# Kernel tuning notes

Measured on AMD Instinct MI355X. Metric: run time of the kernel, lower is better.

The kernel has to match this reference:

```python
import jax, jax.numpy as jnp
import numpy as np

EMBED_DIM = 512
SMOOTH = 4.0        # args.lambda_softmax
LAMBDA_LSE = 6.0    # args.lambda_lse
LEAKY_SLOPE = 0.1
EPS = 1e-8


def setup_inputs() -> dict:
    key = jax.random.key(0)
    k1, k2, k3 = jax.random.split(key, 3)
    n_contract, n_region = 32, 256
    n_law, max_len = 32, 256
    contracts = jax.random.normal(k1, (n_contract, n_region, EMBED_DIM), jnp.float32)
    laws = jax.random.normal(k2, (n_law, max_len, EMBED_DIM), jnp.float32)
    law_lens = jax.random.randint(k3, (n_law,), 128, max_len + 1, jnp.int32)
    return {"contracts": contracts, "laws": laws, "law_lens": law_lens}


def reference(contracts, laws, law_lens):
    # contracts: [C, R, D], laws: [N, L, D], law_lens: [N]
    n_law, max_len, d = laws.shape
    # mask[n, l] = 1 if word l is within law n's true length
    mask = (jnp.arange(max_len)[None, :] < law_lens[:, None]).astype(contracts.dtype)

    # attn = law @ contract^T / sqrt(D): [N, C, L, R]
    attn = jnp.einsum('nld,crd->nclr', laws, contracts) / jnp.sqrt(jnp.float32(d))
    attn = jax.nn.leaky_relu(attn, LEAKY_SLOPE)
    # l2norm over region dim (per law-word row)
    attn = attn / (jnp.linalg.norm(attn, axis=-1, keepdims=True) + EPS)
    attn = jax.nn.softmax(attn, axis=-1) * SMOOTH
    # zero out contributions from padded law words (ragged lengths)
    attn = attn * mask[:, None, :, None]

    # weighted_law: [N, C, R, D]
    wlaw = jnp.einsum('nld,nclr->ncrd', laws, attn)

    # cosine similarity along D: [N, C, R]
    w12 = jnp.sum(contracts[None] * wlaw, axis=-1)
    w1 = jnp.linalg.norm(contracts, axis=-1)[None]          # [1, C, R]
    w2 = jnp.linalg.norm(wlaw, axis=-1)                      # [N, C, R]
    sim = w12 / jnp.maximum(w1 * w2, EPS)

    # LogSumExp aggregation over regions -> [N, C]
    row_sim = jnp.log(jnp.sum(jnp.exp(sim * LAMBDA_LSE), axis=-1)) / LAMBDA_LSE
    # concatenate per-law columns -> [C, N]
    return row_sim.T
```

## Files before the change

### kernel.cpp

```cpp
#include <hip/hip_runtime.h>
#include <hip/hip_bf16.h>

#define CN 32
#define RN 256
#define DN 512
#define NN 32
#define LN 256

#define STAGE_OFF 131072
#define SMEM_TOTAL 163840

typedef short v8s __attribute__((ext_vector_type(8)));
typedef float v4f __attribute__((ext_vector_type(4)));
typedef const __attribute__((address_space(1))) void* gas1_t;
typedef __attribute__((address_space(3))) void* las3_t;

__device__ __forceinline__ void gl2lds16(const void* g, void* l) {
  __builtin_amdgcn_global_load_lds((gas1_t)g, (las3_t)l, 16, 0, 0);
}

__device__ __forceinline__ unsigned short f2bf(float x) {
  unsigned int u = __float_as_uint(x);
  u = (u + 0x7fffu + ((u >> 16) & 1u)) >> 16;
  return (unsigned short)u;
}
__device__ __forceinline__ float bf2f(unsigned short h) {
  return __uint_as_float(((unsigned int)h) << 16);
}

__device__ __forceinline__ const v8s* stgFrag(const unsigned short* buf, int r,
                                              int quad) {
  return (const v8s*)(buf + r * 32 + ((quad ^ ((r >> 1) & 3)) << 3));
}

__device__ __forceinline__ int satIdx(int r, int col) {
  return (r << 8) | ((((col >> 3) ^ (r & 7)) << 3) | (col & 7));
}

__global__ __launch_bounds__(256) void prep_kernel(
    const float* __restrict__ con, const float* __restrict__ laws,
    unsigned short* __restrict__ lawsB, unsigned short* __restrict__ conB,
    float* __restrict__ cnorm) {
  const int b = blockIdx.x;
  const int t = threadIdx.x;
  const int base = b * DN;
  float a0 = laws[base + t], a1 = laws[base + t + 256];
  lawsB[base + t] = f2bf(a0);
  lawsB[base + t + 256] = f2bf(a1);
  float c0 = con[base + t], c1 = con[base + t + 256];
  conB[base + t] = f2bf(c0);
  conB[base + t + 256] = f2bf(c1);
  float s = c0 * c0 + c1 * c1;
#pragma unroll
  for (int m = 1; m < 64; m <<= 1) s += __shfl_xor(s, m, 64);
  __shared__ float r4[4];
  if ((t & 63) == 0) r4[t >> 6] = s;
  __syncthreads();
  if (t == 0) cnorm[b] = sqrtf(r4[0] + r4[1] + r4[2] + r4[3]);
}

__global__ __launch_bounds__(512) void gramm_kernel(
    const unsigned short* __restrict__ lawsB, unsigned short* __restrict__ G) {
  __shared__ unsigned short lawsAll[256 * 32];
  __shared__ unsigned short lawsSub[64 * 32];
  const int bx = blockIdx.x;
  const int n = bx >> 2;
  const int m0 = (bx & 3) << 6;
  const int t = threadIdx.x;
  const int lane = t & 63;
  const int w = t >> 6;
  const int quad = lane >> 4;
  const int l16 = lane & 15;
  const int sub = t & 3;
  const int rQ = t >> 2;
  const int subx = sub ^ ((rQ >> 1) & 3);
  const unsigned short* lawN = lawsB + n * (LN * DN);
  const int wr = (w & 1) << 5;
  const int wc = (w >> 1) << 6;

  v4f acc[2][4];
#pragma unroll
  for (int a = 0; a < 2; ++a)
#pragma unroll
    for (int b = 0; b < 4; ++b) acc[a][b] = (v4f){0.f, 0.f, 0.f, 0.f};

  for (int ch = 0; ch < 16; ++ch) {
    const int dk = ch << 5;
    __syncthreads();
#pragma unroll
    for (int i = 0; i < 2; ++i)
      gl2lds16(lawN + (i * 128 + rQ) * DN + dk + subx * 8,
               (char*)lawsAll + i * 8192 + t * 16);
    if (t < 256)
      gl2lds16(lawN + (m0 + rQ) * DN + dk + subx * 8, (char*)lawsSub + t * 16);
    __syncthreads();
    v8s af0 = *stgFrag(lawsSub, wr + l16, quad);
    v8s af1 = *stgFrag(lawsSub, wr + 16 + l16, quad);
#pragma unroll
    for (int rt = 0; rt < 4; ++rt) {
      v8s bf = *stgFrag(lawsAll, wc + rt * 16 + l16, quad);
      acc[0][rt] = __builtin_amdgcn_mfma_f32_16x16x32_bf16(af0, bf, acc[0][rt], 0, 0, 0);
      acc[1][rt] = __builtin_amdgcn_mfma_f32_16x16x32_bf16(af1, bf, acc[1][rt], 0, 0, 0);
    }
  }
  unsigned short* g = G + n * (LN * LN);
#pragma unroll
  for (int tl = 0; tl < 2; ++tl)
#pragma unroll
    for (int reg = 0; reg < 4; ++reg) {
      const int l = m0 + wr + tl * 16 + quad * 4 + reg;
#pragma unroll
      for (int rt = 0; rt < 4; ++rt)
        g[l * LN + wc + rt * 16 + l16] = f2bf(acc[tl][rt][reg]);
    }
}

__global__ __launch_bounds__(512, 2) void main_kernel(
    const int* __restrict__ law_lens, const unsigned short* __restrict__ lawsB,
    const unsigned short* __restrict__ conB, const unsigned short* __restrict__ Gm,
    const float* __restrict__ cnorm, float* __restrict__ out) {
  extern __shared__ char smem[];
  unsigned short* sAt = (unsigned short*)smem;
  char* stage = smem + STAGE_OFF;

  const int bid = blockIdx.x;
  const int n = bid >> 5;
  const int c = bid & 31;
  const int t = threadIdx.x;
  const int lane = t & 63;
  const int w = t >> 6;
  const int quad = lane >> 4;
  const int l16 = lane & 15;
  const int sub = t & 3;
  const int rQ = t >> 2;
  const int subx = sub ^ ((rQ >> 1) & 3);
  const int len = law_lens[n];

  const unsigned short* lawN = lawsB + n * (LN * DN);
  const unsigned short* conC = conB + c * (RN * DN);
  const unsigned short* Gn = Gm + n * (LN * LN);

  unsigned short* conS = (unsigned short*)stage;
  unsigned short* lawsS = (unsigned short*)(stage + 16384);

  float w12p[16];
#pragma unroll
  for (int i = 0; i < 16; ++i) w12p[i] = 0.f;

  {
    v4f acc[2][16];
#pragma unroll
    for (int a = 0; a < 2; ++a)
#pragma unroll
      for (int b = 0; b < 16; ++b) acc[a][b] = (v4f){0.f, 0.f, 0.f, 0.f};

    for (int ch = 0; ch < 16; ++ch) {
      const int dk = ch << 5;
      __syncthreads();
#pragma unroll
      for (int i = 0; i < 2; ++i)
        gl2lds16(conC + (i * 128 + rQ) * DN + dk + subx * 8,
                 (char*)conS + i * 8192 + t * 16);
#pragma unroll
      for (int i = 0; i < 2; ++i)
        gl2lds16(lawN + (i * 128 + rQ) * DN + dk + subx * 8,
                 (char*)lawsS + i * 8192 + t * 16);
      __syncthreads();
      v8s af0 = *stgFrag(lawsS, w * 32 + l16, quad);
      v8s af1 = *stgFrag(lawsS, w * 32 + 16 + l16, quad);
#pragma unroll
      for (int rt = 0; rt < 16; ++rt) {
        v8s bf = *stgFrag(conS, rt * 16 + l16, quad);
        acc[0][rt] = __builtin_amdgcn_mfma_f32_16x16x32_bf16(af0, bf, acc[0][rt], 0, 0, 0);
        acc[1][rt] = __builtin_amdgcn_mfma_f32_16x16x32_bf16(af1, bf, acc[1][rt], 0, 0, 0);
      }
    }
#pragma unroll
    for (int tl = 0; tl < 2; ++tl) {
      unsigned int pk[16][2];
#pragma unroll
      for (int reg = 0; reg < 4; ++reg) {
        const int lg = w * 32 + tl * 16 + quad * 4 + reg;
        float v[16], lv[16];
        float ss = 0.f, mx = -1e30f;
#pragma unroll
        for (int rt = 0; rt < 16; ++rt) {
          v[rt] = acc[tl][rt][reg] * 0.04419417382415922f;
          lv[rt] = v[rt] > 0.f ? v[rt] : 0.1f * v[rt];
          ss += lv[rt] * lv[rt];
          mx = fmaxf(mx, lv[rt]);
        }
#pragma unroll
        for (int m = 1; m < 16; m <<= 1) {
          ss += __shfl_xor(ss, m, 64);
          mx = fmaxf(mx, __shfl_xor(mx, m, 64));
        }
        const float inv = 1.f / (sqrtf(ss) + 1e-8f);
        const float xm = mx * inv;
        float e[16];
        float den = 0.f;
#pragma unroll
        for (int rt = 0; rt < 16; ++rt) {
          e[rt] = __expf(lv[rt] * inv - xm);
          den += e[rt];
        }
#pragma unroll
        for (int m = 1; m < 16; m <<= 1) den += __shfl_xor(den, m, 64);
        const float sc = (lg < len) ? 4.f / den : 0.f;
#pragma unroll
        for (int rt = 0; rt < 16; ++rt) {
          const float a = e[rt] * sc;
          w12p[rt] += a * v[rt];
          const unsigned int h = f2bf(a);
          if (reg & 1)
            pk[rt][reg >> 1] |= h << 16;
          else
            pk[rt][reg >> 1] = h;
        }
      }
      const int lg0 = w * 32 + tl * 16 + quad * 4;
#pragma unroll
      for (int rt = 0; rt < 16; ++rt)
        *(uint2*)(sAt + satIdx(rt * 16 + l16, lg0)) = *(uint2*)pk[rt];
    }
  }
#pragma unroll
  for (int rt = 0; rt < 16; ++rt) {
    w12p[rt] += __shfl_xor(w12p[rt], 16, 64);
    w12p[rt] += __shfl_xor(w12p[rt], 32, 64);
  }

  unsigned short* Gs = (unsigned short*)stage;
  float nsv[2][4];
  {
    v4f acc[2][16];
#pragma unroll
    for (int a = 0; a < 2; ++a)
#pragma unroll
      for (int b = 0; b < 16; ++b) acc[a][b] = (v4f){0.f, 0.f, 0.f, 0.f};

    for (int ch = 0; ch < 8; ++ch) {
      const int lk = ch << 5;
      __syncthreads();
#pragma unroll
      for (int i = 0; i < 2; ++i)
        gl2lds16(Gn + (i * 128 + rQ) * LN + lk + subx * 8,
                 (char*)Gs + i * 8192 + t * 16);
      __syncthreads();
      v8s af0 = *(const v8s*)(sAt + satIdx(w * 32 + l16, lk + quad * 8));
      v8s af1 = *(const v8s*)(sAt + satIdx(w * 32 + 16 + l16, lk + quad * 8));
#pragma unroll
      for (int lt = 0; lt < 16; ++lt) {
        v8s bf = *stgFrag(Gs, lt * 16 + l16, quad);
        acc[0][lt] = __builtin_amdgcn_mfma_f32_16x16x32_bf16(af0, bf, acc[0][lt], 0, 0, 0);
        acc[1][lt] = __builtin_amdgcn_mfma_f32_16x16x32_bf16(af1, bf, acc[1][lt], 0, 0, 0);
      }
    }
#pragma unroll
    for (int tl = 0; tl < 2; ++tl) {
#pragma unroll
      for (int reg = 0; reg < 4; ++reg) {
        const int r = w * 32 + tl * 16 + quad * 4 + reg;
        float s = 0.f;
#pragma unroll
        for (int lt = 0; lt < 16; ++lt)
          s += acc[tl][lt][reg] * bf2f(sAt[satIdx(r, lt * 16 + l16)]);
#pragma unroll
        for (int m = 1; m < 16; m <<= 1) s += __shfl_xor(s, m, 64);
        nsv[tl][reg] = s;
      }
    }
  }

  float* w12s = (float*)stage;
  float* nsqS = (float*)(stage + 8192);
  float* red = (float*)(stage + 9216);
  __syncthreads();
  if (l16 == 0) {
#pragma unroll
    for (int tl = 0; tl < 2; ++tl)
#pragma unroll
      for (int reg = 0; reg < 4; ++reg)
        nsqS[w * 32 + tl * 16 + quad * 4 + reg] = nsv[tl][reg];
  }
  if (lane < 16) {
#pragma unroll
    for (int rt = 0; rt < 16; ++rt) w12s[w * 256 + rt * 16 + lane] = w12p[rt];
  }
  __syncthreads();
  float p = 0.f;
  if (t < 256) {
    float w12 = 0.f;
#pragma unroll
    for (int i = 0; i < 8; ++i) w12 += w12s[i * 256 + t];
    const float w1 = cnorm[c * RN + t];
    const float w2 = sqrtf(fmaxf(nsqS[t], 0.f));
    const float sim = (w12 * 22.627416997969522f) / fmaxf(w1 * w2, 1e-8f);
    p = __expf(6.f * sim);
  }
#pragma unroll
  for (int m = 1; m < 64; m <<= 1) p += __shfl_xor(p, m, 64);
  __syncthreads();
  if (lane == 0) red[w] = p;
  __syncthreads();
  if (t == 0) {
    float s = 0.f;
#pragma unroll
    for (int i = 0; i < 8; ++i) s += red[i];
    out[c * NN + n] = logf(s) / 6.f;
  }
}

extern "C" void kernel_launch(void* const* d_in, const int* in_sizes, int n_in,
                              void* d_out, int out_size, void* d_ws, size_t ws_size,
                              hipStream_t stream) {
  (void)in_sizes; (void)n_in; (void)out_size;
  const float* contracts = (const float*)d_in[0];
  const float* laws = (const float*)d_in[1];
  const int* law_lens = (const int*)d_in[2];
  float* out = (float*)d_out;

  unsigned short* lawsB = (unsigned short*)d_ws;
  unsigned short* conB = lawsB + NN * LN * DN;
  unsigned short* G = conB + CN * RN * DN;
  float* cnorm = (float*)(G + NN * LN * LN);
  if (ws_size < (size_t)21004288) return;

  hipFuncSetAttribute((const void*)main_kernel,
                      hipFuncAttributeMaxDynamicSharedMemorySize, SMEM_TOTAL);

  prep_kernel<<<8192, 256, 0, stream>>>(contracts, laws, lawsB, conB, cnorm);
  gramm_kernel<<<128, 512, 0, stream>>>(lawsB, G);
  main_kernel<<<1024, 512, SMEM_TOTAL, stream>>>(law_lens, lawsB, conB, G, cnorm, out);
}
```

Measured before the change: 250.3 us.

## Load MFMA operands directly from global memory instead of LDS staging

Drops the global_load_lds staging buffers and their per-chunk barriers in the Gram and main kernels. Each wave now loads its A and B bf16 fragments straight from global memory into registers, with loops unrolled by two so loads can overlap the MFMAs. The prep kernel is also rewritten to use float4 loads and packed 16-byte bf16 stores, with one wave per contract row for the norms. The cost is that all 8 waves of a block now fetch the same B fragments separately, which multiplies L1/L2 traffic and raises register pressure in exchange for removing the synchronization.

```diff
diff --git a/kernel.cpp b/kernel.cpp
--- a/kernel.cpp
+++ b/kernel.cpp
@@ -7,17 +7,11 @@
 #define NN 32
 #define LN 256
 
-#define STAGE_OFF 131072
-#define SMEM_TOTAL 163840
+#define RED_BASE 131072
+#define SMEM_TOTAL (131072 + 9216 + 64)
 
 typedef short v8s __attribute__((ext_vector_type(8)));
 typedef float v4f __attribute__((ext_vector_type(4)));
-typedef const __attribute__((address_space(1))) void* gas1_t;
-typedef __attribute__((address_space(3))) void* las3_t;
-
-__device__ __forceinline__ void gl2lds16(const void* g, void* l) {
-  __builtin_amdgcn_global_load_lds((gas1_t)g, (las3_t)l, 16, 0, 0);
-}
 
 __device__ __forceinline__ unsigned short f2bf(float x) {
   unsigned int u = __float_as_uint(x);
@@ -28,11 +22,6 @@
   return __uint_as_float(((unsigned int)h) << 16);
 }
 
-__device__ __forceinline__ const v8s* stgFrag(const unsigned short* buf, int r,
-                                              int quad) {
-  return (const v8s*)(buf + r * 32 + ((quad ^ ((r >> 1) & 3)) << 3));
-}
-
 __device__ __forceinline__ int satIdx(int r, int col) {
   return (r << 8) | ((((col >> 3) ^ (r & 7)) << 3) | (col & 7));
 }
@@ -41,28 +30,35 @@
     const float* __restrict__ con, const float* __restrict__ laws,
     unsigned short* __restrict__ lawsB, unsigned short* __restrict__ conB,
     float* __restrict__ cnorm) {
-  const int b = blockIdx.x;
+  const int bid = blockIdx.x;
   const int t = threadIdx.x;
-  const int base = b * DN;
-  float a0 = laws[base + t], a1 = laws[base + t + 256];
-  lawsB[base + t] = f2bf(a0);
-  lawsB[base + t + 256] = f2bf(a1);
-  float c0 = con[base + t], c1 = con[base + t + 256];
-  conB[base + t] = f2bf(c0);
-  conB[base + t + 256] = f2bf(c1);
-  float s = c0 * c0 + c1 * c1;
-#pragma unroll
-  for (int m = 1; m < 64; m <<= 1) s += __shfl_xor(s, m, 64);
-  __shared__ float r4[4];
-  if ((t & 63) == 0) r4[t >> 6] = s;
-  __syncthreads();
-  if (t == 0) cnorm[b] = sqrtf(r4[0] + r4[1] + r4[2] + r4[3]);
+  if (bid < 2048) {
+    const int r = bid * 4 + (t >> 6);
+    const int lane = t & 63;
+    const float4* src = (const float4*)(con + r * DN + lane * 8);
+    float4 x0 = src[0], x1 = src[1];
+    unsigned short h[8];
+    h[0] = f2bf(x0.x); h[1] = f2bf(x0.y); h[2] = f2bf(x0.z); h[3] = f2bf(x0.w);
+    h[4] = f2bf(x1.x); h[5] = f2bf(x1.y); h[6] = f2bf(x1.z); h[7] = f2bf(x1.w);
+    *(v8s*)(conB + r * DN + lane * 8) = *(v8s*)h;
+    float s = x0.x * x0.x + x0.y * x0.y + x0.z * x0.z + x0.w * x0.w +
+              x1.x * x1.x + x1.y * x1.y + x1.z * x1.z + x1.w * x1.w;
+#pragma unroll
+    for (int m = 1; m < 64; m <<= 1) s += __shfl_xor(s, m, 64);
+    if (lane == 0) cnorm[r] = sqrtf(s);
+  } else {
+    const int off = (bid - 2048) * 2048 + t * 8;
+    const float4* src = (const float4*)(laws + off);
+    float4 x0 = src[0], x1 = src[1];
+    unsigned short h[8];
+    h[0] = f2bf(x0.x); h[1] = f2bf(x0.y); h[2] = f2bf(x0.z); h[3] = f2bf(x0.w);
+    h[4] = f2bf(x1.x); h[5] = f2bf(x1.y); h[6] = f2bf(x1.z); h[7] = f2bf(x1.w);
+    *(v8s*)(lawsB + off) = *(v8s*)h;
+  }
 }
 
 __global__ __launch_bounds__(512) void gramm_kernel(
     const unsigned short* __restrict__ lawsB, unsigned short* __restrict__ G) {
-  __shared__ unsigned short lawsAll[256 * 32];
-  __shared__ unsigned short lawsSub[64 * 32];
   const int bx = blockIdx.x;
   const int n = bx >> 2;
   const int m0 = (bx & 3) << 6;
@@ -71,36 +67,33 @@
   const int w = t >> 6;
   const int quad = lane >> 4;
   const int l16 = lane & 15;
-  const int sub = t & 3;
-  const int rQ = t >> 2;
-  const int subx = sub ^ ((rQ >> 1) & 3);
   const unsigned short* lawN = lawsB + n * (LN * DN);
   const int wr = (w & 1) << 5;
   const int wc = (w >> 1) << 6;
 
+  const unsigned short* a0p = lawN + (m0 + wr + l16) * DN + quad * 8;
+  const unsigned short* a1p = a0p + 16 * DN;
+  const unsigned short* bp = lawN + (wc + l16) * DN + quad * 8;
+
   v4f acc[2][4];
 #pragma unroll
   for (int a = 0; a < 2; ++a)
 #pragma unroll
     for (int b = 0; b < 4; ++b) acc[a][b] = (v4f){0.f, 0.f, 0.f, 0.f};
 
+#pragma unroll 2
   for (int ch = 0; ch < 16; ++ch) {
     const int dk = ch << 5;
-    __syncthreads();
-#pragma unroll
-    for (int i = 0; i < 2; ++i)
-      gl2lds16(lawN + (i * 128 + rQ) * DN + dk + subx * 8,
-               (char*)lawsAll + i * 8192 + t * 16);
-    if (t < 256)
-      gl2lds16(lawN + (m0 + rQ) * DN + dk + subx * 8, (char*)lawsSub + t * 16);
-    __syncthreads();
-    v8s af0 = *stgFrag(lawsSub, wr + l16, quad);
-    v8s af1 = *stgFrag(lawsSub, wr + 16 + l16, quad);
+    v8s af0 = *(const v8s*)(a0p + dk);
+    v8s af1 = *(const v8s*)(a1p + dk);
+    v8s bfr[4];
+#pragma unroll
+    for (int rt = 0; rt < 4; ++rt)
+      bfr[rt] = *(const v8s*)(bp + rt * (16 * DN) + dk);
 #pragma unroll
     for (int rt = 0; rt < 4; ++rt) {
-      v8s bf = *stgFrag(lawsAll, wc + rt * 16 + l16, quad);
-      acc[0][rt] = __builtin_amdgcn_mfma_f32_16x16x32_bf16(af0, bf, acc[0][rt], 0, 0, 0);
-      acc[1][rt] = __builtin_amdgcn_mfma_f32_16x16x32_bf16(af1, bf, acc[1][rt], 0, 0, 0);
+      acc[0][rt] = __builtin_amdgcn_mfma_f32_16x16x32_bf16(af0, bfr[rt], acc[0][rt], 0, 0, 0);
+      acc[1][rt] = __builtin_amdgcn_mfma_f32_16x16x32_bf16(af1, bfr[rt], acc[1][rt], 0, 0, 0);
     }
   }
   unsigned short* g = G + n * (LN * LN);
@@ -121,7 +114,6 @@
     const float* __restrict__ cnorm, float* __restrict__ out) {
   extern __shared__ char smem[];
   unsigned short* sAt = (unsigned short*)smem;
-  char* stage = smem + STAGE_OFF;
 
   const int bid = blockIdx.x;
   const int n = bid >> 5;
@@ -131,48 +123,40 @@
   const int w = t >> 6;
   const int quad = lane >> 4;
   const int l16 = lane & 15;
-  const int sub = t & 3;
-  const int rQ = t >> 2;
-  const int subx = sub ^ ((rQ >> 1) & 3);
   const int len = law_lens[n];
 
   const unsigned short* lawN = lawsB + n * (LN * DN);
   const unsigned short* conC = conB + c * (RN * DN);
   const unsigned short* Gn = Gm + n * (LN * LN);
 
-  unsigned short* conS = (unsigned short*)stage;
-  unsigned short* lawsS = (unsigned short*)(stage + 16384);
-
   float w12p[16];
 #pragma unroll
   for (int i = 0; i < 16; ++i) w12p[i] = 0.f;
 
   {
+    const unsigned short* a0p = lawN + (w * 32 + l16) * DN + quad * 8;
+    const unsigned short* a1p = a0p + 16 * DN;
+    const unsigned short* bp = conC + l16 * DN + quad * 8;
+
     v4f acc[2][16];
 #pragma unroll
     for (int a = 0; a < 2; ++a)
 #pragma unroll
       for (int b = 0; b < 16; ++b) acc[a][b] = (v4f){0.f, 0.f, 0.f, 0.f};
 
+#pragma unroll 2
     for (int ch = 0; ch < 16; ++ch) {
       const int dk = ch << 5;
-      __syncthreads();
-#pragma unroll
-      for (int i = 0; i < 2; ++i)
-        gl2lds16(conC + (i * 128 + rQ) * DN + dk + subx * 8,
-                 (char*)conS + i * 8192 + t * 16);
-#pragma unroll
-      for (int i = 0; i < 2; ++i)
-        gl2lds16(lawN + (i * 128 + rQ) * DN + dk + subx * 8,
-                 (char*)lawsS + i * 8192 + t * 16);
-      __syncthreads();
-      v8s af0 = *stgFrag(lawsS, w * 32 + l16, quad);
-      v8s af1 = *stgFrag(lawsS, w * 32 + 16 + l16, quad);
+      v8s af0 = *(const v8s*)(a0p + dk);
+      v8s af1 = *(const v8s*)(a1p + dk);
+      v8s bfr[16];
+#pragma unroll
+      for (int rt = 0; rt < 16; ++rt)
+        bfr[rt] = *(const v8s*)(bp + rt * (16 * DN) + dk);
 #pragma unroll
       for (int rt = 0; rt < 16; ++rt) {
-        v8s bf = *stgFrag(conS, rt * 16 + l16, quad);
-        acc[0][rt] = __builtin_amdgcn_mfma_f32_16x16x32_bf16(af0, bf, acc[0][rt], 0, 0, 0);
-        acc[1][rt] = __builtin_amdgcn_mfma_f32_16x16x32_bf16(af1, bf, acc[1][rt], 0, 0, 0);
+        acc[0][rt] = __builtin_amdgcn_mfma_f32_16x16x32_bf16(af0, bfr[rt], acc[0][rt], 0, 0, 0);
+        acc[1][rt] = __builtin_amdgcn_mfma_f32_16x16x32_bf16(af1, bfr[rt], acc[1][rt], 0, 0, 0);
       }
     }
 #pragma unroll
@@ -230,30 +214,30 @@
     w12p[rt] += __shfl_xor(w12p[rt], 32, 64);
   }
 
-  unsigned short* Gs = (unsigned short*)stage;
+  __syncthreads();
+
   float nsv[2][4];
   {
+    const unsigned short* gp = Gn + l16 * LN + quad * 8;
     v4f acc[2][16];
 #pragma unroll
     for (int a = 0; a < 2; ++a)
 #pragma unroll
       for (int b = 0; b < 16; ++b) acc[a][b] = (v4f){0.f, 0.f, 0.f, 0.f};
 
+#pragma unroll 2
     for (int ch = 0; ch < 8; ++ch) {
       const int lk = ch << 5;
-      __syncthreads();
-#pragma unroll
-      for (int i = 0; i < 2; ++i)
-        gl2lds16(Gn + (i * 128 + rQ) * LN + lk + subx * 8,
-                 (char*)Gs + i * 8192 + t * 16);
-      __syncthreads();
       v8s af0 = *(const v8s*)(sAt + satIdx(w * 32 + l16, lk + quad * 8));
       v8s af1 = *(const v8s*)(sAt + satIdx(w * 32 + 16 + l16, lk + quad * 8));
+      v8s bfr[16];
+#pragma unroll
+      for (int lt = 0; lt < 16; ++lt)
+        bfr[lt] = *(const v8s*)(gp + lt * (16 * LN) + lk);
 #pragma unroll
       for (int lt = 0; lt < 16; ++lt) {
-        v8s bf = *stgFrag(Gs, lt * 16 + l16, quad);
-        acc[0][lt] = __builtin_amdgcn_mfma_f32_16x16x32_bf16(af0, bf, acc[0][lt], 0, 0, 0);
-        acc[1][lt] = __builtin_amdgcn_mfma_f32_16x16x32_bf16(af1, bf, acc[1][lt], 0, 0, 0);
+        acc[0][lt] = __builtin_amdgcn_mfma_f32_16x16x32_bf16(af0, bfr[lt], acc[0][lt], 0, 0, 0);
+        acc[1][lt] = __builtin_amdgcn_mfma_f32_16x16x32_bf16(af1, bfr[lt], acc[1][lt], 0, 0, 0);
       }
     }
 #pragma unroll
@@ -272,10 +256,9 @@
     }
   }
 
-  float* w12s = (float*)stage;
-  float* nsqS = (float*)(stage + 8192);
-  float* red = (float*)(stage + 9216);
-  __syncthreads();
+  float* w12s = (float*)(smem + RED_BASE);
+  float* nsqS = (float*)(smem + RED_BASE + 8192);
+  float* red = (float*)(smem + RED_BASE + 9216);
   if (l16 == 0) {
 #pragma unroll
     for (int tl = 0; tl < 2; ++tl)
@@ -300,7 +283,6 @@
   }
 #pragma unroll
   for (int m = 1; m < 64; m <<= 1) p += __shfl_xor(p, m, 64);
-  __syncthreads();
   if (lane == 0) red[w] = p;
   __syncthreads();
   if (t == 0) {
@@ -329,7 +311,7 @@
   hipFuncSetAttribute((const void*)main_kernel,
                       hipFuncAttributeMaxDynamicSharedMemorySize, SMEM_TOTAL);
 
-  prep_kernel<<<8192, 256, 0, stream>>>(contracts, laws, lawsB, conB, cnorm);
+  prep_kernel<<<4096, 256, 0, stream>>>(contracts, laws, lawsB, conB, cnorm);
   gramm_kernel<<<128, 512, 0, stream>>>(lawsB, G);
   main_kernel<<<1024, 512, SMEM_TOTAL, stream>>>(law_lens, lawsB, conB, G, cnorm, out);
 }
```

After: 515.7 us. 106% more time.

## Double-buffer LDS staging, widen main kernel to 1024 threads, vectorize prep

Applied to the files above, without the earlier changes.

The main kernel now runs 1024 threads, with each wave owning 16 law rows instead of 32. Law A-fragments are read straight from global memory rather than staged in LDS. Contract and Gram tiles are double-buffered, so the next chunk's load is issued before the current MFMAs, which removes one barrier per step. Softmax recomputes the exponentials instead of holding them in registers and drops max-subtraction, which is safe because L2-normalised inputs are bounded. The prep kernel uses vectorized float4 loads with separate block ranges for contracts and laws. The risks are register pressure under the new 1024-thread launch bound, and the loss of the old design where all waves shared the law tile in LDS.

```diff
diff --git a/kernel.cpp b/kernel.cpp
--- a/kernel.cpp
+++ b/kernel.cpp
@@ -41,22 +41,31 @@
     const float* __restrict__ con, const float* __restrict__ laws,
     unsigned short* __restrict__ lawsB, unsigned short* __restrict__ conB,
     float* __restrict__ cnorm) {
-  const int b = blockIdx.x;
+  const int bid = blockIdx.x;
   const int t = threadIdx.x;
-  const int base = b * DN;
-  float a0 = laws[base + t], a1 = laws[base + t + 256];
-  lawsB[base + t] = f2bf(a0);
-  lawsB[base + t + 256] = f2bf(a1);
-  float c0 = con[base + t], c1 = con[base + t + 256];
-  conB[base + t] = f2bf(c0);
-  conB[base + t + 256] = f2bf(c1);
-  float s = c0 * c0 + c1 * c1;
-#pragma unroll
-  for (int m = 1; m < 64; m <<= 1) s += __shfl_xor(s, m, 64);
-  __shared__ float r4[4];
-  if ((t & 63) == 0) r4[t >> 6] = s;
-  __syncthreads();
-  if (t == 0) cnorm[b] = sqrtf(r4[0] + r4[1] + r4[2] + r4[3]);
+  if (bid < 2048) {
+    const int r = bid * 4 + (t >> 6);
+    const int lane = t & 63;
+    const float4* src = (const float4*)(con + r * DN + lane * 8);
+    float4 x0 = src[0], x1 = src[1];
+    unsigned short h[8];
+    h[0] = f2bf(x0.x); h[1] = f2bf(x0.y); h[2] = f2bf(x0.z); h[3] = f2bf(x0.w);
+    h[4] = f2bf(x1.x); h[5] = f2bf(x1.y); h[6] = f2bf(x1.z); h[7] = f2bf(x1.w);
+    *(v8s*)(conB + r * DN + lane * 8) = *(v8s*)h;
+    float s = x0.x * x0.x + x0.y * x0.y + x0.z * x0.z + x0.w * x0.w +
+              x1.x * x1.x + x1.y * x1.y + x1.z * x1.z + x1.w * x1.w;
+#pragma unroll
+    for (int m = 1; m < 64; m <<= 1) s += __shfl_xor(s, m, 64);
+    if (lane == 0) cnorm[r] = sqrtf(s);
+  } else {
+    const int off = (bid - 2048) * 2048 + t * 8;
+    const float4* src = (const float4*)(laws + off);
+    float4 x0 = src[0], x1 = src[1];
+    unsigned short h[8];
+    h[0] = f2bf(x0.x); h[1] = f2bf(x0.y); h[2] = f2bf(x0.z); h[3] = f2bf(x0.w);
+    h[4] = f2bf(x1.x); h[5] = f2bf(x1.y); h[6] = f2bf(x1.z); h[7] = f2bf(x1.w);
+    *(v8s*)(lawsB + off) = *(v8s*)h;
+  }
 }
 
 __global__ __launch_bounds__(512) void gramm_kernel(
@@ -115,7 +124,7 @@
     }
 }
 
-__global__ __launch_bounds__(512, 2) void main_kernel(
+__global__ __launch_bounds__(1024, 4) void main_kernel(
     const int* __restrict__ law_lens, const unsigned short* __restrict__ lawsB,
     const unsigned short* __restrict__ conB, const unsigned short* __restrict__ Gm,
     const float* __restrict__ cnorm, float* __restrict__ out) {
@@ -140,148 +149,124 @@
   const unsigned short* conC = conB + c * (RN * DN);
   const unsigned short* Gn = Gm + n * (LN * LN);
 
-  unsigned short* conS = (unsigned short*)stage;
-  unsigned short* lawsS = (unsigned short*)(stage + 16384);
-
   float w12p[16];
 #pragma unroll
   for (int i = 0; i < 16; ++i) w12p[i] = 0.f;
 
   {
-    v4f acc[2][16];
-#pragma unroll
-    for (int a = 0; a < 2; ++a)
-#pragma unroll
-      for (int b = 0; b < 16; ++b) acc[a][b] = (v4f){0.f, 0.f, 0.f, 0.f};
+    const unsigned short* a0p = lawN + (w * 16 + l16) * DN + quad * 8;
+
+    v4f acc[16];
+#pragma unroll
+    for (int b = 0; b < 16; ++b) acc[b] = (v4f){0.f, 0.f, 0.f, 0.f};
+
+    gl2lds16(conC + rQ * DN + subx * 8, stage + t * 16);
 
     for (int ch = 0; ch < 16; ++ch) {
       const int dk = ch << 5;
       __syncthreads();
-#pragma unroll
-      for (int i = 0; i < 2; ++i)
-        gl2lds16(conC + (i * 128 + rQ) * DN + dk + subx * 8,
-                 (char*)conS + i * 8192 + t * 16);
-#pragma unroll
-      for (int i = 0; i < 2; ++i)
-        gl2lds16(lawN + (i * 128 + rQ) * DN + dk + subx * 8,
-                 (char*)lawsS + i * 8192 + t * 16);
-      __syncthreads();
-      v8s af0 = *stgFrag(lawsS, w * 32 + l16, quad);
-      v8s af1 = *stgFrag(lawsS, w * 32 + 16 + l16, quad);
+      v8s af = *(const v8s*)(a0p + dk);
+      __builtin_amdgcn_sched_barrier(0);
+      if (ch < 15)
+        gl2lds16(conC + rQ * DN + (dk + 32) + subx * 8,
+                 stage + ((ch + 1) & 1) * 16384 + t * 16);
+      __builtin_amdgcn_sched_barrier(0);
+      const unsigned short* cs =
+          (const unsigned short*)(stage + (ch & 1) * 16384);
 #pragma unroll
       for (int rt = 0; rt < 16; ++rt) {
-        v8s bf = *stgFrag(conS, rt * 16 + l16, quad);
-        acc[0][rt] = __builtin_amdgcn_mfma_f32_16x16x32_bf16(af0, bf, acc[0][rt], 0, 0, 0);
-        acc[1][rt] = __builtin_amdgcn_mfma_f32_16x16x32_bf16(af1, bf, acc[1][rt], 0, 0, 0);
-      }
-    }
-#pragma unroll
-    for (int tl = 0; tl < 2; ++tl) {
-      unsigned int pk[16][2];
-#pragma unroll
-      for (int reg = 0; reg < 4; ++reg) {
-        const int lg = w * 32 + tl * 16 + quad * 4 + reg;
-        float v[16], lv[16];
-        float ss = 0.f, mx = -1e30f;
-#pragma unroll
-        for (int rt = 0; rt < 16; ++rt) {
-          v[rt] = acc[tl][rt][reg] * 0.04419417382415922f;
-          lv[rt] = v[rt] > 0.f ? v[rt] : 0.1f * v[rt];
-          ss += lv[rt] * lv[rt];
-          mx = fmaxf(mx, lv[rt]);
-        }
-#pragma unroll
-        for (int m = 1; m < 16; m <<= 1) {
-          ss += __shfl_xor(ss, m, 64);
-          mx = fmaxf(mx, __shfl_xor(mx, m, 64));
-        }
-        const float inv = 1.f / (sqrtf(ss) + 1e-8f);
-        const float xm = mx * inv;
-        float e[16];
-        float den = 0.f;
-#pragma unroll
-        for (int rt = 0; rt < 16; ++rt) {
-          e[rt] = __expf(lv[rt] * inv - xm);
-          den += e[rt];
-        }
-#pragma unroll
-        for (int m = 1; m < 16; m <<= 1) den += __shfl_xor(den, m, 64);
-        const float sc = (lg < len) ? 4.f / den : 0.f;
-#pragma unroll
-        for (int rt = 0; rt < 16; ++rt) {
-          const float a = e[rt] * sc;
-          w12p[rt] += a * v[rt];
-          const unsigned int h = f2bf(a);
-          if (reg & 1)
-            pk[rt][reg >> 1] |= h << 16;
-          else
-            pk[rt][reg >> 1] = h;
-        }
-      }
-      const int lg0 = w * 32 + tl * 16 + quad * 4;
-#pragma unroll
-      for (int rt = 0; rt < 16; ++rt)
-        *(uint2*)(sAt + satIdx(rt * 16 + l16, lg0)) = *(uint2*)pk[rt];
-    }
-  }
+        v8s bf = *stgFrag(cs, rt * 16 + l16, quad);
+        acc[rt] = __builtin_amdgcn_mfma_f32_16x16x32_bf16(af, bf, acc[rt], 0, 0, 0);
+      }
+    }
+#pragma unroll
+    for (int reg = 0; reg < 4; ++reg) {
+      const int lg = w * 16 + quad * 4 + reg;
+      float ss = 0.f;
+#pragma unroll
+      for (int rt = 0; rt < 16; ++rt) {
+        const float v = acc[rt][reg] * 0.04419417382415922f;
+        const float lv = v > 0.f ? v : 0.1f * v;
+        ss += lv * lv;
+      }
+#pragma unroll
+      for (int m = 1; m < 16; m <<= 1) ss += __shfl_xor(ss, m, 64);
+      const float inv = 1.f / (sqrtf(ss) + 1e-8f);
+      float den = 0.f;
+#pragma unroll
+      for (int rt = 0; rt < 16; ++rt) {
+        const float v = acc[rt][reg] * 0.04419417382415922f;
+        const float lv = v > 0.f ? v : 0.1f * v;
+        den += __expf(lv * inv);
+      }
+#pragma unroll
+      for (int m = 1; m < 16; m <<= 1) den += __shfl_xor(den, m, 64);
+      const float sc = (lg < len) ? 4.f / den : 0.f;
+#pragma unroll
+      for (int rt = 0; rt < 16; ++rt) {
+        const float v = acc[rt][reg] * 0.04419417382415922f;
+        const float lv = v > 0.f ? v : 0.1f * v;
+        const float a = __expf(lv * inv) * sc;
+        w12p[rt] += a * v;
+        sAt[satIdx(rt * 16 + l16, lg)] = f2bf(a);
+      }
+    }
+  }
+
+  __syncthreads();
+
+  gl2lds16(Gn + rQ * LN + subx * 8, stage + t * 16);
+
 #pragma unroll
   for (int rt = 0; rt < 16; ++rt) {
     w12p[rt] += __shfl_xor(w12p[rt], 16, 64);
     w12p[rt] += __shfl_xor(w12p[rt], 32, 64);
   }
 
-  unsigned short* Gs = (unsigned short*)stage;
-  float nsv[2][4];
+  float nsv[4];
   {
-    v4f acc[2][16];
-#pragma unroll
-    for (int a = 0; a < 2; ++a)
-#pragma unroll
-      for (int b = 0; b < 16; ++b) acc[a][b] = (v4f){0.f, 0.f, 0.f, 0.f};
+    v4f acc[16];
+#pragma unroll
+    for (int b = 0; b < 16; ++b) acc[b] = (v4f){0.f, 0.f, 0.f, 0.f};
 
     for (int ch = 0; ch < 8; ++ch) {
       const int lk = ch << 5;
       __syncthreads();
-#pragma unroll
-      for (int i = 0; i < 2; ++i)
-        gl2lds16(Gn + (i * 128 + rQ) * LN + lk + subx * 8,
-                 (char*)Gs + i * 8192 + t * 16);
-      __syncthreads();
-      v8s af0 = *(const v8s*)(sAt + satIdx(w * 32 + l16, lk + quad * 8));
-      v8s af1 = *(const v8s*)(sAt + satIdx(w * 32 + 16 + l16, lk + quad * 8));
+      v8s af = *(const v8s*)(sAt + satIdx(w * 16 + l16, lk + quad * 8));
+      __builtin_amdgcn_sched_barrier(0);
+      if (ch < 7)
+        gl2lds16(Gn + rQ * LN + (lk + 32) + subx * 8,
+                 stage + ((ch + 1) & 1) * 16384 + t * 16);
+      __builtin_amdgcn_sched_barrier(0);
+      const unsigned short* gs =
+          (const unsigned short*)(stage + (ch & 1) * 16384);
 #pragma unroll
       for (int lt = 0; lt < 16; ++lt) {
-        v8s bf = *stgFrag(Gs, lt * 16 + l16, quad);
-        acc[0][lt] = __builtin_amdgcn_mfma_f32_16x16x32_bf16(af0, bf, acc[0][lt], 0, 0, 0);
-        acc[1][lt] = __builtin_amdgcn_mfma_f32_16x16x32_bf16(af1, bf, acc[1][lt], 0, 0, 0);
-      }
-    }
-#pragma unroll
-    for (int tl = 0; tl < 2; ++tl) {
-#pragma unroll
-      for (int reg = 0; reg < 4; ++reg) {
-        const int r = w * 32 + tl * 16 + quad * 4 + reg;
-        float s = 0.f;
-#pragma unroll
-        for (int lt = 0; lt < 16; ++lt)
-          s += acc[tl][lt][reg] * bf2f(sAt[satIdx(r, lt * 16 + l16)]);
-#pragma unroll
-        for (int m = 1; m < 16; m <<= 1) s += __shfl_xor(s, m, 64);
-        nsv[tl][reg] = s;
-      }
+        v8s bf = *stgFrag(gs, lt * 16 + l16, quad);
+        acc[lt] = __builtin_amdgcn_mfma_f32_16x16x32_bf16(af, bf, acc[lt], 0, 0, 0);
+      }
+    }
+#pragma unroll
+    for (int reg = 0; reg < 4; ++reg) {
+      const int r = w * 16 + quad * 4 + reg;
+      float s = 0.f;
+#pragma unroll
+      for (int lt = 0; lt < 16; ++lt)
+        s += acc[lt][reg] * bf2f(sAt[satIdx(r, lt * 16 + l16)]);
+#pragma unroll
+      for (int m = 1; m < 16; m <<= 1) s += __shfl_xor(s, m, 64);
+      nsv[reg] = s;
     }
   }
 
   float* w12s = (float*)stage;
-  float* nsqS = (float*)(stage + 8192);
-  float* red = (float*)(stage + 9216);
+  float* nsqS = (float*)(stage + 16384);
+  float* red = (float*)(stage + 17408);
   __syncthreads();
   if (l16 == 0) {
 #pragma unroll
-    for (int tl = 0; tl < 2; ++tl)
-#pragma unroll
-      for (int reg = 0; reg < 4; ++reg)
-        nsqS[w * 32 + tl * 16 + quad * 4 + reg] = nsv[tl][reg];
+    for (int reg = 0; reg < 4; ++reg)
+      nsqS[w * 16 + quad * 4 + reg] = nsv[reg];
   }
   if (lane < 16) {
 #pragma unroll
@@ -292,7 +277,7 @@
   if (t < 256) {
     float w12 = 0.f;
 #pragma unroll
-    for (int i = 0; i < 8; ++i) w12 += w12s[i * 256 + t];
+    for (int i = 0; i < 16; ++i) w12 += w12s[i * 256 + t];
     const float w1 = cnorm[c * RN + t];
     const float w2 = sqrtf(fmaxf(nsqS[t], 0.f));
     const float sim = (w12 * 22.627416997969522f) / fmaxf(w1 * w2, 1e-8f);
@@ -300,14 +285,10 @@
   }
 #pragma unroll
   for (int m = 1; m < 64; m <<= 1) p += __shfl_xor(p, m, 64);
-  __syncthreads();
-  if (lane == 0) red[w] = p;
+  if (t < 256 && lane == 0) red[w] = p;
   __syncthreads();
   if (t == 0) {
-    float s = 0.f;
-#pragma unroll
-    for (int i = 0; i < 8; ++i) s += red[i];
-    out[c * NN + n] = logf(s) / 6.f;
+    out[c * NN + n] = logf(red[0] + red[1] + red[2] + red[3]) / 6.f;
   }
 }
 
@@ -329,7 +310,8 @@
   hipFuncSetAttribute((const void*)main_kernel,
                       hipFuncAttributeMaxDynamicSharedMemorySize, SMEM_TOTAL);
 
-  prep_kernel<<<8192, 256, 0, stream>>>(contracts, laws, lawsB, conB, cnorm);
+  prep_kernel<<<4096, 256, 0, stream>>>(contracts, laws, lawsB, conB, cnorm);
   gramm_kernel<<<128, 512, 0, stream>>>(lawsB, G);
-  main_kernel<<<1024, 512, SMEM_TOTAL, stream>>>(law_lens, lawsB, conB, G, cnorm, out);
-}
+  main_kernel<<<1024, 1024, SMEM_TOTAL, stream>>>(law_lens, lawsB, conB, G,
+                                                  cnorm, out);
+}
```

Result: no change. 249.6 us (-0.3%).
